# Kernel tuning notes

Measured on AMD Instinct MI355X. Metric: run time of the kernel, lower is better.

## Reference

```python
import jax, jax.numpy as jnp
import numpy as np
from jax import lax


def _conv(x, w, b):
    # x: [B,C,H,W], w: [O,I,3,3] (OIHW), SAME padding, stride 1
    y = lax.conv_general_dilated(x, w, (1, 1), 'SAME',
                                 dimension_numbers=('NCHW', 'OIHW', 'NCHW'))
    return y + b[None, :, None, None]


def _maxpool2(x):
    return lax.reduce_window(x, -jnp.inf, lax.max, (1, 1, 2, 2), (1, 1, 2, 2), 'VALID')


def setup_inputs() -> dict:
    key = jax.random.key(0)
    ks = iter(jax.random.split(key, 40))

    def conv_w(o, i):
        std = np.sqrt(2.0 / (9.0 * o)).astype(np.float32)  # kaiming as in _initialize_weights
        return jax.random.normal(next(ks), (o, i, 3, 3), jnp.float32) * std

    def lin_w(o, i):
        return jax.random.normal(next(ks), (o, i), jnp.float32) * 0.01

    inp = {
        'x': jax.random.normal(next(ks), (64, 3, 64, 64), jnp.float32),
        'y': jax.random.randint(next(ks), (64,), 0, 1000, dtype=jnp.int32),
        'b_table': jax.random.randint(next(ks), (1000, 128), 0, 512, dtype=jnp.int32),
        'cw0': conv_w(64, 3),    'cb0': jnp.zeros((64,), jnp.float32),
        'cw1': conv_w(128, 64),  'cb1': jnp.zeros((128,), jnp.float32),
        'cw2a': conv_w(256, 128), 'cb2a': jnp.zeros((256,), jnp.float32),
        'cw2b': conv_w(256, 256), 'cb2b': jnp.zeros((256,), jnp.float32),
        'cw3a': conv_w(512, 256), 'cb3a': jnp.zeros((512,), jnp.float32),
        'cw3b': conv_w(512, 512), 'cb3b': jnp.zeros((512,), jnp.float32),
        'cw4a': conv_w(512, 512), 'cb4a': jnp.zeros((512,), jnp.float32),
        'cw4b': conv_w(512, 512), 'cb4b': jnp.zeros((512,), jnp.float32),
        'fw1': lin_w(4096, 2048), 'fb1': jnp.zeros((4096,), jnp.float32),
        'fw2': lin_w(4096, 4096), 'fb2': jnp.zeros((4096,), jnp.float32),
        'fw3': lin_w(1000, 4096), 'fb3': jnp.zeros((1000,), jnp.float32),
    }
    return inp


def reference(x, y, b_table, cw0, cb0, cw1, cb1, cw2a, cb2a, cw2b, cb2b,
              cw3a, cb3a, cw3b, cb3b, cw4a, cb4a, cw4b, cb4b,
              fw1, fb1, fw2, fb2, fw3, fb3):
    B = x.shape[0]
    relu = jax.nn.relu
    # block0 (single conv, relu applied in forward)
    h = relu(_conv(x, cw0, cb0))
    h = _maxpool2(h)                       # 32x32
    # block1
    h = relu(_conv(h, cw1, cb1))
    h = _maxpool2(h)                       # 16x16
    # block2: conv, relu, conv (trailing relu stripped, applied in forward)
    h = relu(_conv(relu(_conv(h, cw2a, cb2a)), cw2b, cb2b))
    h = _maxpool2(h)                       # 8x8
    # block3
    h = relu(_conv(relu(_conv(h, cw3a, cb3a)), cw3b, cb3b))
    h = _maxpool2(h)                       # h==64 path: pool3 -> 4x4
    # block4
    h = relu(_conv(relu(_conv(h, cw4a, cb4a)), cw4b, cb4b))  # [B,512,4,4]

    # ---- engram channel masking (gather + sort + scatter) ----
    ranking = jnp.sort(b_table[y], axis=-1)            # [B, engram_number] channel ids
    mask = jnp.zeros((B, 512), h.dtype).at[jnp.arange(B)[:, None], ranking].set(1.0)
    h = h * mask[:, :, None, None]

    h = _maxpool2(h)                       # [B,512,2,2]
    h = h.reshape(B, -1)                   # [B,2048]
    # classifier (dropout = identity in eval mode)
    h = relu(h @ fw1.T + fb1)
    h = relu(h @ fw2.T + fb2)
    return h @ fw3.T + fb3                 # [B,1000]
```

## Files before the change

kernel.cpp:

```cpp
#include <hip/hip_runtime.h>
#include <hip/hip_bf16.h>
#include <cstddef>

typedef __attribute__((ext_vector_type(8))) short short8;
typedef __attribute__((ext_vector_type(4))) float fx4;
typedef __attribute__((ext_vector_type(4))) unsigned short us4;
typedef __attribute__((ext_vector_type(8))) unsigned short us8;

constexpr int BATCH = 64;

static __device__ __forceinline__ unsigned short f2bf(float x) {
    __hip_bfloat16 h = __float2bfloat16(x);
    return *reinterpret_cast<unsigned short*>(&h);
}

__global__ __launch_bounds__(256)
void conv0_kernel(const float* __restrict__ x, const float* __restrict__ w,
                  const float* __restrict__ bias, unsigned short* __restrict__ out)
{
    __shared__ float ins[3][18][19];
    const int tid  = threadIdx.x;
    const int lane = tid & 63;
    const int wv   = __builtin_amdgcn_readfirstlane(tid >> 6);
    const int img  = blockIdx.x >> 4;
    const int tile = blockIdx.x & 15;
    const int ty0  = (tile >> 2) * 16, tx0 = (tile & 3) * 16;
    const int py0  = (lane >> 3) * 2,  px0 = (lane & 7) * 2;
    const int co0  = wv * 16;

    for (int t = tid; t < 3*18*18; t += 256) {
        int xx = t % 18, yy = (t/18) % 18, ci = t/(18*18);
        int gy = ty0 + yy - 1, gx = tx0 + xx - 1;
        float v = 0.f;
        if (gy >= 0 && gy < 64 && gx >= 0 && gx < 64)
            v = x[((img*3 + ci)*64 + gy)*64 + gx];
        ins[ci][yy][xx] = v;
    }
    __syncthreads();

    float acc[16][4];
    #pragma unroll
    for (int j = 0; j < 16; j++)
        #pragma unroll
        for (int r = 0; r < 4; r++) acc[j][r] = 0.f;

    #pragma unroll
    for (int ci = 0; ci < 3; ci++) {
        float p[4][4];
        #pragma unroll
        for (int dy = 0; dy < 4; dy++)
            #pragma unroll
            for (int dx = 0; dx < 4; dx++)
                p[dy][dx] = ins[ci][py0+dy][px0+dx];
        #pragma unroll
        for (int j = 0; j < 16; j++) {
            const float* wp = w + ((co0+j)*3 + ci)*9;
            float w0=wp[0],w1=wp[1],w2=wp[2],w3=wp[3],w4=wp[4],
                  w5=wp[5],w6=wp[6],w7=wp[7],w8=wp[8];
            #pragma unroll
            for (int oy = 0; oy < 2; oy++)
                #pragma unroll
                for (int ox = 0; ox < 2; ox++)
                    acc[j][oy*2+ox] +=
                        p[oy+0][ox+0]*w0 + p[oy+0][ox+1]*w1 + p[oy+0][ox+2]*w2 +
                        p[oy+1][ox+0]*w3 + p[oy+1][ox+1]*w4 + p[oy+1][ox+2]*w5 +
                        p[oy+2][ox+0]*w6 + p[oy+2][ox+1]*w7 + p[oy+2][ox+2]*w8;
        }
    }

    us8 v0, v1;
    #pragma unroll
    for (int j = 0; j < 16; j++) {
        float m = fmaxf(fmaxf(acc[j][0], acc[j][1]), fmaxf(acc[j][2], acc[j][3]));
        unsigned short u = f2bf(fmaxf(m + bias[co0+j], 0.f));
        if (j < 8) v0[j] = u; else v1[j-8] = u;
    }
    int oy = (ty0+py0) >> 1, ox = (tx0+px0) >> 1;
    unsigned short* o = &out[((size_t)(img*32+oy)*32 + ox)*64 + co0];
    *(us8*)(o)     = v0;
    *(us8*)(o + 8) = v1;
}

struct PPAll {
    const float* src[7];
    unsigned long long dstoff[7];
    int cin[7];
    int cout[7];
    int end[7];
};

__global__ __launch_bounds__(256)
void prepack(PPAll a, unsigned short* __restrict__ wpbase)
{
    int t = blockIdx.x*256 + threadIdx.x;
    if (t >= 1024000) return;
    int l = 0;
    while (t >= a.end[l]) l++;
    int start = (l == 0) ? 0 : a.end[l-1];
    int local = t - start;
    int cin = a.cin[l], cout = a.cout[l];
    int co = local / cin, ci = local % cin;
    const float* s = a.src[l] + (size_t)local * 9;
    unsigned short* d = wpbase + a.dstoff[l];
    int kct = cin >> 5;
    #pragma unroll
    for (int k = 0; k < 9; k++)
        d[((size_t)(k*kct + (ci >> 5))*cout + co)*32 + (ci & 31)] = f2bf(s[k]);
}

template<int CIN, int COUT, int H, int CW, int SW, int P, int KS, bool POOL>
__global__ __launch_bounds__(256, 2)
void conv_mfma(const unsigned short* __restrict__ in, const unsigned short* __restrict__ wp,
               const float* __restrict__ bias, void* __restrict__ outp)
{
    constexpr int RY   = (P == 1) ? 8 : 4;
    constexpr int HY   = RY + 2, HX = RY + 2;
    constexpr int KCT  = CIN / 32;
    constexpr int CINS = CIN / KS;
    constexpr int KC   = CINS / 32;
    constexpr int PADW = (CINS == 128) ? 24 : 8;
    constexpr int STR  = CINS + PADW;
    constexpr int REG  = (P == 1) ? (H/8)*(H/8) : 1;
    static_assert(CW * SW == 4, "4 waves");

    __shared__ unsigned short ins[SW][P][HY][HX][STR];

    const int tid  = threadIdx.x;
    const int lane = tid & 63;
    const int wv   = __builtin_amdgcn_readfirstlane(tid >> 6);
    const int quad = lane >> 4;
    const int nn   = lane & 15;
    const int cg   = wv % CW;
    const int sg   = wv / CW;
    const int co0  = (blockIdx.y * CW + cg) * 64;
    const int ks   = (KS > 1) ? (int)blockIdx.z : 0;

    auto decode = [&](int rg, int& img, int& y0, int& x0) {
        if constexpr (P == 1) {
            img = rg / REG;
            int rs = rg % REG;
            constexpr int RXN = (P == 1) ? (H/8) : 1;
            y0 = (rs / RXN) * 8;
            x0 = (rs % RXN) * 8;
        } else {
            img = rg * 4; y0 = 0; x0 = 0;
        }
    };

    int w_img, w_y0, w_x0;
    decode(blockIdx.x * SW + sg, w_img, w_y0, w_x0);

    {
        constexpr int E = SW*P*HY*HX*(CINS/8);
        for (int u = tid; u < E; u += 256) {
            int q   = u % (CINS/8);
            int pix = u / (CINS/8);
            int xx  = pix % HX;
            int yy  = (pix / HX) % HY;
            int pp  = (pix / (HX*HY)) % P;
            int ss  = pix / (HX*HY*P);
            int s_img, s_y0, s_x0;
            decode(blockIdx.x * SW + ss, s_img, s_y0, s_x0);
            int gy = s_y0 + yy - 1, gx = s_x0 + xx - 1;
            int imgp = s_img + ((P == 1) ? 0 : pp);
            us8 v;
            #pragma unroll
            for (int e = 0; e < 8; e++) v[e] = 0;
            if (gy >= 0 && gy < H && gx >= 0 && gx < H)
                v = *(const us8*)&in[(((size_t)imgp*H + gy)*H + gx)*CIN + ks*CINS + q*8];
            *(us8*)&ins[ss][pp][yy][xx][q*8] = v;
        }
    }
    __syncthreads();

    fx4 acc[4][4];
    #pragma unroll
    for (int mf = 0; mf < 4; mf++)
        #pragma unroll
        for (int nf = 0; nf < 4; nf++) {
            fx4 z = {0.f, 0.f, 0.f, 0.f};
            acc[mf][nf] = z;
        }

    #pragma unroll 1
    for (int kc = 0; kc < KC; kc++) {
        #pragma unroll 3
        for (int tap = 0; tap < 9; tap++) {
            const int dy = tap / 3, dx = tap % 3;
            const unsigned short* wb =
                wp + ((size_t)(tap*KCT + ks*KC + kc)*COUT + co0 + nn)*32 + quad*8;
            short8 a[4];
            #pragma unroll
            for (int mf = 0; mf < 4; mf++)
                a[mf] = *(const short8*)(wb + (size_t)mf*16*32);
            short8 b[4];
            #pragma unroll
            for (int nf = 0; nf < 4; nf++) {
                int pp, py, px;
                if constexpr (P == 1) { pp = 0;  py = (nf>>1)*4 + (nn>>2); px = (nf&1)*4 + (nn&3); }
                else                  { pp = nf; py = (nn>>2);             px = (nn&3); }
                b[nf] = *(const short8*)&ins[sg][pp][py+dy][px+dx][kc*32 + quad*8];
            }
            #pragma unroll
            for (int mf = 0; mf < 4; mf++)
                #pragma unroll
                for (int nf = 0; nf < 4; nf++)
                    acc[mf][nf] = __builtin_amdgcn_mfma_f32_16x16x32_bf16(
                        a[mf], b[nf], acc[mf][nf], 0, 0, 0);
        }
    }

    if constexpr (KS > 1) {
        float* part = (float*)outp;
        constexpr size_t NPIX = (size_t)BATCH * H * H;
        #pragma unroll
        for (int mf = 0; mf < 4; mf++)
            #pragma unroll
            for (int nf = 0; nf < 4; nf++) {
                int img, py, px;
                if constexpr (P == 1) { img = w_img;      py = w_y0 + (nf>>1)*4 + (nn>>2); px = w_x0 + (nf&1)*4 + (nn&3); }
                else                  { img = w_img + nf; py = (nn>>2);                    px = (nn&3); }
                size_t npix = (size_t)img*H*H + py*H + px;
                size_t idx  = ((size_t)ks*NPIX + npix)*COUT + co0 + mf*16 + quad*4;
                *(fx4*)&part[idx] = acc[mf][nf];
            }
    } else if constexpr (POOL) {
        unsigned short* out = (unsigned short*)outp;
        constexpr int HO = H/2;
        #pragma unroll
        for (int mf = 0; mf < 4; mf++) {
            fx4 b4 = *(const fx4*)&bias[co0 + mf*16 + quad*4];
            #pragma unroll
            for (int nf = 0; nf < 4; nf++) {
                us4 o;
                #pragma unroll
                for (int r = 0; r < 4; r++) {
                    float v = acc[mf][nf][r];
                    v = fmaxf(v, __shfl_xor(v, 1));
                    v = fmaxf(v, __shfl_xor(v, 4));
                    o[r] = f2bf(fmaxf(v + b4[r], 0.f));
                }
                if ((nn & 5) == 0) {
                    int py = w_y0 + (nf>>1)*4 + (nn>>2);
                    int px = w_x0 + (nf&1)*4 + (nn&3);
                    size_t idx = (((size_t)w_img*HO + (py>>1))*HO + (px>>1))*COUT
                               + co0 + mf*16 + quad*4;
                    *(us4*)&out[idx] = o;
                }
            }
        }
    } else {
        unsigned short* out = (unsigned short*)outp;
        #pragma unroll
        for (int mf = 0; mf < 4; mf++) {
            fx4 b4 = *(const fx4*)&bias[co0 + mf*16 + quad*4];
            #pragma unroll
            for (int nf = 0; nf < 4; nf++) {
                us4 o;
                #pragma unroll
                for (int r = 0; r < 4; r++)
                    o[r] = f2bf(fmaxf(acc[mf][nf][r] + b4[r], 0.f));
                int py = w_y0 + (nf>>1)*4 + (nn>>2);
                int px = w_x0 + (nf&1)*4 + (nn&3);
                size_t idx = (((size_t)w_img*H + py)*H + px)*COUT + co0 + mf*16 + quad*4;
                *(us4*)&out[idx] = o;
            }
        }
    }
}

template<int KS, int NPIX, int CO>
__global__ __launch_bounds__(256)
void combine_nhwc(const float* __restrict__ part, const float* __restrict__ bias,
                  unsigned short* __restrict__ out)
{
    constexpr int C4 = CO/4;
    int t = blockIdx.x*256 + threadIdx.x;
    if (t >= NPIX*C4) return;
    int c4 = t % C4, pix = t / C4;
    fx4 s = *(const fx4*)&bias[c4*4];
    #pragma unroll
    for (int k = 0; k < KS; k++)
        s += *(const fx4*)&part[((size_t)k*NPIX + pix)*CO + c4*4];
    us4 o;
    #pragma unroll
    for (int r = 0; r < 4; r++) o[r] = f2bf(fmaxf(s[r], 0.f));
    *(us4*)&out[(size_t)pix*CO + c4*4] = o;
}

template<int KS, int HI, int CO>
__global__ __launch_bounds__(256)
void combine_pool(const float* __restrict__ part, const float* __restrict__ bias,
                  unsigned short* __restrict__ out)
{
    constexpr int HO = HI/2, C4 = CO/4;
    constexpr size_t NPIX = (size_t)BATCH*HI*HI;
    int t = blockIdx.x*256 + threadIdx.x;
    if (t >= BATCH*HO*HO*C4) return;
    int c4 = t % C4;
    int r  = t / C4;
    int xo = r % HO, yo = (r/HO) % HO, img = r/(HO*HO);
    fx4 m = {-1e30f, -1e30f, -1e30f, -1e30f};
    #pragma unroll
    for (int iy = 0; iy < 2; iy++)
        #pragma unroll
        for (int ix = 0; ix < 2; ix++) {
            size_t pix = (size_t)img*HI*HI + (2*yo+iy)*HI + (2*xo+ix);
            fx4 s = {0.f,0.f,0.f,0.f};
            #pragma unroll
            for (int k = 0; k < KS; k++)
                s += *(const fx4*)&part[((size_t)k*NPIX + pix)*CO + c4*4];
            #pragma unroll
            for (int e = 0; e < 4; e++) m[e] = fmaxf(m[e], s[e]);
        }
    fx4 b4 = *(const fx4*)&bias[c4*4];
    us4 o;
    #pragma unroll
    for (int e = 0; e < 4; e++) o[e] = f2bf(fmaxf(m[e] + b4[e], 0.f));
    *(us4*)&out[((size_t)(img*HO+yo)*HO + xo)*CO + c4*4] = o;
}

__global__ __launch_bounds__(256)
void combine4b(const float* __restrict__ part, const float* __restrict__ bias,
               const float* __restrict__ mask, unsigned short* __restrict__ X0)
{
    int t = blockIdx.x*256 + threadIdx.x;
    if (t >= BATCH*512) return;
    int b = t / 512, c = t % 512;
    float s[16];
    #pragma unroll
    for (int p = 0; p < 16; p++) s[p] = 0.f;
    #pragma unroll
    for (int k = 0; k < 16; k++)
        #pragma unroll
        for (int p = 0; p < 16; p++)
            s[p] += part[((size_t)k*1024 + b*16 + p)*512 + c];
    float mk = mask[b*512 + c], bb = bias[c];
    us4 o;
    #pragma unroll
    for (int py = 0; py < 2; py++)
        #pragma unroll
        for (int px = 0; px < 2; px++) {
            float m = fmaxf(fmaxf(s[(2*py)*4 + 2*px],     s[(2*py)*4 + 2*px+1]),
                            fmaxf(s[(2*py+1)*4 + 2*px],   s[(2*py+1)*4 + 2*px+1]));
            o[py*2+px] = f2bf(mk * fmaxf(m + bb, 0.f));
        }
    *(us4*)&X0[(size_t)b*2048 + c*4] = o;
}

__global__ void build_mask(const int* __restrict__ y, const int* __restrict__ btab,
                           float* __restrict__ mask)
{
    __shared__ float m[512];
    int b = blockIdx.x;
    int t = threadIdx.x;
    for (int i = t; i < 512; i += 128) m[i] = 0.f;
    __syncthreads();
    int cls = y[b];
    int idx = btab[cls*128 + t];
    m[idx] = 1.0f;
    __syncthreads();
    for (int i = t; i < 512; i += 128) mask[b*512 + i] = m[i];
}

template<int K, int NP, int NREAL, int KSO>
__global__ __launch_bounds__(256)
void fc_mfma(const unsigned short* __restrict__ X, const float* __restrict__ W,
             float* __restrict__ P)
{
    constexpr int KW = K / (KSO*4);
    constexpr int NI = KW / 32;
    __shared__ alignas(16) unsigned short XL[4][64][40];
    __shared__ alignas(16) float R[64][68];

    const int tid  = threadIdx.x;
    const int lane = tid & 63;
    const int wv   = __builtin_amdgcn_readfirstlane(tid >> 6);
    const int quad = lane >> 4;
    const int nn   = lane & 15;
    const int c0   = blockIdx.x * 64;
    const int ksb  = blockIdx.y;
    const int k0   = (ksb*4 + wv) * KW;

    fx4 acc[4][4];
    #pragma unroll
    for (int mf = 0; mf < 4; mf++)
        #pragma unroll
        for (int nf = 0; nf < 4; nf++) {
            fx4 z = {0.f,0.f,0.f,0.f};
            acc[mf][nf] = z;
        }

    #pragma unroll
    for (int kc = 0; kc < NI; kc++) {
        const int kw = k0 + kc*32;
        const unsigned short* xp = X + (size_t)lane*K + kw;
        us8 x0 = *(const us8*)(xp);
        us8 x1 = *(const us8*)(xp + 8);
        us8 x2 = *(const us8*)(xp + 16);
        us8 x3 = *(const us8*)(xp + 24);
        *(us8*)&XL[wv][lane][0]  = x0;
        *(us8*)&XL[wv][lane][8]  = x1;
        *(us8*)&XL[wv][lane][16] = x2;
        *(us8*)&XL[wv][lane][24] = x3;
        short8 b[4];
        #pragma unroll
        for (int nf = 0; nf < 4; nf++) {
            int c = c0 + nf*16 + nn;
            if (c > NREAL-1) c = NREAL-1;
            const float* wp = W + (size_t)c*K + kw + quad*8;
            float4 f0 = *(const float4*)(wp);
            float4 f1 = *(const float4*)(wp + 4);
            short8 t;
            t[0] = (short)f2bf(f0.x); t[1] = (short)f2bf(f0.y);
            t[2] = (short)f2bf(f0.z); t[3] = (short)f2bf(f0.w);
            t[4] = (short)f2bf(f1.x); t[5] = (short)f2bf(f1.y);
            t[6] = (short)f2bf(f1.z); t[7] = (short)f2bf(f1.w);
            b[nf] = t;
        }
        short8 a[4];
        #pragma unroll
        for (int mf = 0; mf < 4; mf++)
            a[mf] = *(const short8*)&XL[wv][mf*16 + nn][quad*8];
        #pragma unroll
        for (int mf = 0; mf < 4; mf++)
            #pragma unroll
            for (int nf = 0; nf < 4; nf++)
                acc[mf][nf] = __builtin_amdgcn_mfma_f32_16x16x32_bf16(
                    a[mf], b[nf], acc[mf][nf], 0, 0, 0);
    }

    for (int ww = 0; ww < 4; ww++) {
        __syncthreads();
        if (wv == ww) {
            #pragma unroll
            for (int mf = 0; mf < 4; mf++)
                #pragma unroll
                for (int nf = 0; nf < 4; nf++) {
                    int n = nf*16 + nn;
                    #pragma unroll
                    for (int r = 0; r < 4; r++) {
                        int m = mf*16 + quad*4 + r;
                        float v = acc[mf][nf][r];
                        if (ww) v += R[m][n];
                        R[m][n] = v;
                    }
                }
        }
    }
    __syncthreads();
    {
        int m  = tid >> 2;
        int n0 = (tid & 3) * 16;
        float* dst = P + ((size_t)ksb*64 + m)*NP + c0 + n0;
        #pragma unroll
        for (int j = 0; j < 4; j++) {
            fx4 v = *(const fx4*)&R[m][n0 + j*4];
            *(fx4*)(dst + j*4) = v;
        }
    }
}

template<int N, int KS>
__global__ __launch_bounds__(256)
void fc_combine_bf16(const float* __restrict__ P, const float* __restrict__ bias,
                     unsigned short* __restrict__ Xo)
{
    int t = blockIdx.x*256 + threadIdx.x;
    if (t >= 64*(N/4)) return;
    int c4 = t % (N/4);
    int b  = t / (N/4);
    fx4 s = *(const fx4*)&bias[c4*4];
    #pragma unroll
    for (int ks = 0; ks < KS; ks++)
        s += *(const fx4*)&P[((size_t)ks*64 + b)*N + c4*4];
    us4 o;
    #pragma unroll
    for (int r = 0; r < 4; r++) o[r] = f2bf(fmaxf(s[r], 0.f));
    *(us4*)&Xo[(size_t)b*N + c4*4] = o;
}

__global__ __launch_bounds__(256)
void fc3_combine(const float* __restrict__ P, const float* __restrict__ bias,
                 float* __restrict__ out)
{
    int t = blockIdx.x*256 + threadIdx.x;
    if (t >= 64*1000) return;
    int b = t / 1000, c = t % 1000;
    float s = bias[c];
    #pragma unroll
    for (int ks = 0; ks < 32; ks++)
        s += P[((size_t)ks*64 + b)*1024 + c];
    out[t] = s;
}

extern "C" void kernel_launch(void* const* d_in, const int* in_sizes, int n_in,
                              void* d_out, int out_size, void* d_ws, size_t ws_size,
                              hipStream_t stream)
{
    const float* x    = (const float*)d_in[0];
    const int*   y    = (const int*)  d_in[1];
    const int*   btab = (const int*)  d_in[2];
    const float* cw0  = (const float*)d_in[3];  const float* cb0  = (const float*)d_in[4];
    const float* cw1  = (const float*)d_in[5];  const float* cb1  = (const float*)d_in[6];
    const float* cw2a = (const float*)d_in[7];  const float* cb2a = (const float*)d_in[8];
    const float* cw2b = (const float*)d_in[9];  const float* cb2b = (const float*)d_in[10];
    const float* cw3a = (const float*)d_in[11]; const float* cb3a = (const float*)d_in[12];
    const float* cw3b = (const float*)d_in[13]; const float* cb3b = (const float*)d_in[14];
    const float* cw4a = (const float*)d_in[15]; const float* cb4a = (const float*)d_in[16];
    const float* cw4b = (const float*)d_in[17]; const float* cb4b = (const float*)d_in[18];
    const float* fw1  = (const float*)d_in[19]; const float* fb1  = (const float*)d_in[20];
    const float* fw2  = (const float*)d_in[21]; const float* fb2  = (const float*)d_in[22];
    const float* fw3  = (const float*)d_in[23]; const float* fb3  = (const float*)d_in[24];
    (void)in_sizes; (void)n_in; (void)out_size; (void)ws_size;

    float* ws = (float*)d_ws;
    unsigned short* ActA = (unsigned short*)(ws);
    unsigned short* ActB = (unsigned short*)(ws + 2097152);
    float*          Pp   = ws + 3145728;
    unsigned short* Wp   = (unsigned short*)(ws + 11534336);
    float*          M    = ws + 16142336;
    unsigned short* X0   = (unsigned short*)(ws + 16175104);
    unsigned short* X1   = (unsigned short*)(ws + 16240640);
    unsigned short* X2   = (unsigned short*)(ws + 16371712);

    PPAll pa;
    const float* srcs[7] = {cw1, cw2a, cw2b, cw3a, cw3b, cw4a, cw4b};
    const unsigned long long doffs[7] = {0, 73728, 368640, 958464, 2138112, 4497408, 6856704};
    const int cins[7]  = {64, 128, 256, 256, 512, 512, 512};
    const int couts[7] = {128, 256, 256, 512, 512, 512, 512};
    const int ends[7]  = {8192, 40960, 106496, 237568, 499712, 761856, 1024000};
    for (int i = 0; i < 7; i++) {
        pa.src[i] = srcs[i]; pa.dstoff[i] = doffs[i];
        pa.cin[i] = cins[i]; pa.cout[i] = couts[i]; pa.end[i] = ends[i];
    }
    prepack<<<4000, 256, 0, stream>>>(pa, Wp);

    conv0_kernel<<<1024, 256, 0, stream>>>(x, cw0, cb0, ActA);
    conv_mfma<64,128,32,2,2,1,1,true><<<dim3(512,1,1),256,0,stream>>>(ActA, Wp+0, cb1, ActB);
    conv_mfma<128,256,16,2,2,1,2,false><<<dim3(128,2,2),256,0,stream>>>(ActB, Wp+73728, cb2a, Pp);
    combine_nhwc<2, 16384, 256><<<4096,256,0,stream>>>(Pp, cb2a, ActA);
    conv_mfma<256,256,16,2,2,1,2,false><<<dim3(128,2,2),256,0,stream>>>(ActA, Wp+368640, cb2b, Pp);
    combine_pool<2, 16, 256><<<1024,256,0,stream>>>(Pp, cb2b, ActB);
    conv_mfma<256,512,8,4,1,1,4,false><<<dim3(64,2,4),256,0,stream>>>(ActB, Wp+958464, cb3a, Pp);
    combine_nhwc<4, 4096, 512><<<2048,256,0,stream>>>(Pp, cb3a, ActA);
    conv_mfma<512,512,8,4,1,1,4,false><<<dim3(64,2,4),256,0,stream>>>(ActA, Wp+2138112, cb3b, Pp);
    combine_pool<4, 8, 512><<<512,256,0,stream>>>(Pp, cb3b, ActB);
    conv_mfma<512,512,4,4,1,4,16,false><<<dim3(16,2,16),256,0,stream>>>(ActB, Wp+4497408, cb4a, Pp);
    combine_nhwc<16, 1024, 512><<<512,256,0,stream>>>(Pp, cb4a, ActA);
    build_mask<<<64,128,0,stream>>>(y, btab, M);
    conv_mfma<512,512,4,4,1,4,16,false><<<dim3(16,2,16),256,0,stream>>>(ActA, Wp+6856704, cb4b, Pp);
    combine4b<<<128,256,0,stream>>>(Pp, cb4b, M, X0);
    fc_mfma<2048,4096,4096,8><<<dim3(64,8),256,0,stream>>>(X0, fw1, Pp);
    fc_combine_bf16<4096,8><<<256,256,0,stream>>>(Pp, fb1, X1);
    fc_mfma<4096,4096,4096,8><<<dim3(64,8),256,0,stream>>>(X1, fw2, Pp);
    fc_combine_bf16<4096,8><<<256,256,0,stream>>>(Pp, fb2, X2);
    fc_mfma<4096,1024,1000,32><<<dim3(16,32),256,0,stream>>>(X2, fw3, Pp);
    fc3_combine<<<250,256,0,stream>>>(Pp, fb3, (float*)d_out);
}
```

Before: 516.3 us.

## Halve conv wave tile to 32 pixels, raise occupancy, add split-K pre-reduction

Result: slower. 537.0 us (+4.0%).

```diff
diff --git a/kernel.cpp b/kernel.cpp
--- a/kernel.cpp
+++ b/kernel.cpp
@@ -108,20 +108,19 @@
         d[((size_t)(k*kct + (ci >> 5))*cout + co)*32 + (ci & 31)] = f2bf(s[k]);
 }
 
-template<int CIN, int COUT, int H, int CW, int SW, int P, int KS, bool POOL>
-__global__ __launch_bounds__(256, 2)
+template<int CIN, int COUT, int H, int CW, int SW, int P, int RY, int RX, int KS, bool POOL>
+__global__ __launch_bounds__(256, 4)
 void conv_mfma(const unsigned short* __restrict__ in, const unsigned short* __restrict__ wp,
                const float* __restrict__ bias, void* __restrict__ outp)
 {
-    constexpr int RY   = (P == 1) ? 8 : 4;
-    constexpr int HY   = RY + 2, HX = RY + 2;
+    constexpr int HY   = RY + 2, HX = RX + 2;
     constexpr int KCT  = CIN / 32;
     constexpr int CINS = CIN / KS;
     constexpr int KC   = CINS / 32;
     constexpr int PADW = (CINS == 128) ? 24 : 8;
     constexpr int STR  = CINS + PADW;
-    constexpr int REG  = (P == 1) ? (H/8)*(H/8) : 1;
     static_assert(CW * SW == 4, "4 waves");
+    static_assert(P * RY * RX == 32, "N=32 wave tile");
 
     __shared__ unsigned short ins[SW][P][HY][HX][STR];
 
@@ -137,13 +136,14 @@
 
     auto decode = [&](int rg, int& img, int& y0, int& x0) {
         if constexpr (P == 1) {
+            constexpr int REG = (H/RY)*(H/RX);
+            constexpr int RXN = H/RX;
             img = rg / REG;
             int rs = rg % REG;
-            constexpr int RXN = (P == 1) ? (H/8) : 1;
-            y0 = (rs / RXN) * 8;
-            x0 = (rs % RXN) * 8;
+            y0 = (rs / RXN) * RY;
+            x0 = (rs % RXN) * RX;
         } else {
-            img = rg * 4; y0 = 0; x0 = 0;
+            img = rg * P; y0 = 0; x0 = 0;
         }
     };
 
@@ -173,11 +173,11 @@
     }
     __syncthreads();
 
-    fx4 acc[4][4];
+    fx4 acc[4][2];
     #pragma unroll
     for (int mf = 0; mf < 4; mf++)
         #pragma unroll
-        for (int nf = 0; nf < 4; nf++) {
+        for (int nf = 0; nf < 2; nf++) {
             fx4 z = {0.f, 0.f, 0.f, 0.f};
             acc[mf][nf] = z;
         }
@@ -193,18 +193,18 @@
             #pragma unroll
             for (int mf = 0; mf < 4; mf++)
                 a[mf] = *(const short8*)(wb + (size_t)mf*16*32);
-            short8 b[4];
-            #pragma unroll
-            for (int nf = 0; nf < 4; nf++) {
+            short8 b[2];
+            #pragma unroll
+            for (int nf = 0; nf < 2; nf++) {
                 int pp, py, px;
-                if constexpr (P == 1) { pp = 0;  py = (nf>>1)*4 + (nn>>2); px = (nf&1)*4 + (nn&3); }
-                else                  { pp = nf; py = (nn>>2);             px = (nn&3); }
+                if constexpr (P == 1) { pp = 0;  py = nf*4 + (nn>>2); px = nn & 3; }
+                else                  { pp = nf; py = nn>>2;          px = nn & 3; }
                 b[nf] = *(const short8*)&ins[sg][pp][py+dy][px+dx][kc*32 + quad*8];
             }
             #pragma unroll
             for (int mf = 0; mf < 4; mf++)
                 #pragma unroll
-                for (int nf = 0; nf < 4; nf++)
+                for (int nf = 0; nf < 2; nf++)
                     acc[mf][nf] = __builtin_amdgcn_mfma_f32_16x16x32_bf16(
                         a[mf], b[nf], acc[mf][nf], 0, 0, 0);
         }
@@ -216,10 +216,10 @@
         #pragma unroll
         for (int mf = 0; mf < 4; mf++)
             #pragma unroll
-            for (int nf = 0; nf < 4; nf++) {
+            for (int nf = 0; nf < 2; nf++) {
                 int img, py, px;
-                if constexpr (P == 1) { img = w_img;      py = w_y0 + (nf>>1)*4 + (nn>>2); px = w_x0 + (nf&1)*4 + (nn&3); }
-                else                  { img = w_img + nf; py = (nn>>2);                    px = (nn&3); }
+                if constexpr (P == 1) { img = w_img;      py = w_y0 + nf*4 + (nn>>2); px = w_x0 + (nn&3); }
+                else                  { img = w_img + nf; py = nn>>2;                 px = nn&3; }
                 size_t npix = (size_t)img*H*H + py*H + px;
                 size_t idx  = ((size_t)ks*NPIX + npix)*COUT + co0 + mf*16 + quad*4;
                 *(fx4*)&part[idx] = acc[mf][nf];
@@ -231,7 +231,7 @@
         for (int mf = 0; mf < 4; mf++) {
             fx4 b4 = *(const fx4*)&bias[co0 + mf*16 + quad*4];
             #pragma unroll
-            for (int nf = 0; nf < 4; nf++) {
+            for (int nf = 0; nf < 2; nf++) {
                 us4 o;
                 #pragma unroll
                 for (int r = 0; r < 4; r++) {
@@ -241,9 +241,10 @@
                     o[r] = f2bf(fmaxf(v + b4[r], 0.f));
                 }
                 if ((nn & 5) == 0) {
-                    int py = w_y0 + (nf>>1)*4 + (nn>>2);
-                    int px = w_x0 + (nf&1)*4 + (nn&3);
-                    size_t idx = (((size_t)w_img*HO + (py>>1))*HO + (px>>1))*COUT
+                    int img, py, px;
+                    if constexpr (P == 1) { img = w_img;      py = w_y0 + nf*4 + (nn>>2); px = w_x0 + (nn&3); }
+                    else                  { img = w_img + nf; py = nn>>2;                 px = nn&3; }
+                    size_t idx = (((size_t)img*HO + (py>>1))*HO + (px>>1))*COUT
                                + co0 + mf*16 + quad*4;
                     *(us4*)&out[idx] = o;
                 }
@@ -255,18 +256,34 @@
         for (int mf = 0; mf < 4; mf++) {
             fx4 b4 = *(const fx4*)&bias[co0 + mf*16 + quad*4];
             #pragma unroll
-            for (int nf = 0; nf < 4; nf++) {
+            for (int nf = 0; nf < 2; nf++) {
                 us4 o;
                 #pragma unroll
                 for (int r = 0; r < 4; r++)
                     o[r] = f2bf(fmaxf(acc[mf][nf][r] + b4[r], 0.f));
-                int py = w_y0 + (nf>>1)*4 + (nn>>2);
-                int px = w_x0 + (nf&1)*4 + (nn&3);
-                size_t idx = (((size_t)w_img*H + py)*H + px)*COUT + co0 + mf*16 + quad*4;
+                int img, py, px;
+                if constexpr (P == 1) { img = w_img;      py = w_y0 + nf*4 + (nn>>2); px = w_x0 + (nn&3); }
+                else                  { img = w_img + nf; py = nn>>2;                 px = nn&3; }
+                size_t idx = (((size_t)img*H + py)*H + px)*COUT + co0 + mf*16 + quad*4;
                 *(us4*)&out[idx] = o;
             }
         }
     }
+}
+
+template<int NELEM, int GROUPS, int STRIDE>
+__global__ __launch_bounds__(256)
+void ksum4(float* __restrict__ p)
+{
+    int t = blockIdx.x*256 + threadIdx.x;
+    if (t >= GROUPS*(NELEM/4)) return;
+    int g = t / (NELEM/4);
+    int i = (t % (NELEM/4)) * 4;
+    fx4 s = {0.f,0.f,0.f,0.f};
+    #pragma unroll
+    for (int j = 0; j < 4; j++)
+        s += *(const fx4*)&p[(size_t)((g*4 + j)*STRIDE)*NELEM + i];
+    *(fx4*)&p[(size_t)(g*4*STRIDE)*NELEM + i] = s;
 }
 
 template<int KS, int NPIX, int CO>
@@ -329,12 +346,8 @@
     int b = t / 512, c = t % 512;
     float s[16];
     #pragma unroll
-    for (int p = 0; p < 16; p++) s[p] = 0.f;
-    #pragma unroll
-    for (int k = 0; k < 16; k++)
-        #pragma unroll
-        for (int p = 0; p < 16; p++)
-            s[p] += part[((size_t)k*1024 + b*16 + p)*512 + c];
+    for (int p = 0; p < 16; p++)
+        s[p] = part[(size_t)(b*16 + p)*512 + c];
     float mk = mask[b*512 + c], bb = bias[c];
     us4 o;
     #pragma unroll
@@ -489,8 +502,8 @@
     int b = t / 1000, c = t % 1000;
     float s = bias[c];
     #pragma unroll
-    for (int ks = 0; ks < 32; ks++)
-        s += P[((size_t)ks*64 + b)*1024 + c];
+    for (int ks = 0; ks < 8; ks++)
+        s += P[((size_t)(ks*4)*64 + b)*1024 + c];
     out[t] = s;
 }
 
@@ -537,24 +550,30 @@
     prepack<<<4000, 256, 0, stream>>>(pa, Wp);
 
     conv0_kernel<<<1024, 256, 0, stream>>>(x, cw0, cb0, ActA);
-    conv_mfma<64,128,32,2,2,1,1,true><<<dim3(512,1,1),256,0,stream>>>(ActA, Wp+0, cb1, ActB);
-    conv_mfma<128,256,16,2,2,1,2,false><<<dim3(128,2,2),256,0,stream>>>(ActB, Wp+73728, cb2a, Pp);
+    conv_mfma<64,128,32,2,2,1,8,4,1,true><<<dim3(1024,1,1),256,0,stream>>>(ActA, Wp+0, cb1, ActB);
+    conv_mfma<128,256,16,2,2,1,8,4,2,false><<<dim3(256,2,2),256,0,stream>>>(ActB, Wp+73728, cb2a, Pp);
     combine_nhwc<2, 16384, 256><<<4096,256,0,stream>>>(Pp, cb2a, ActA);
-    conv_mfma<256,256,16,2,2,1,2,false><<<dim3(128,2,2),256,0,stream>>>(ActA, Wp+368640, cb2b, Pp);
+    conv_mfma<256,256,16,2,2,1,8,4,2,false><<<dim3(256,2,2),256,0,stream>>>(ActA, Wp+368640, cb2b, Pp);
     combine_pool<2, 16, 256><<<1024,256,0,stream>>>(Pp, cb2b, ActB);
-    conv_mfma<256,512,8,4,1,1,4,false><<<dim3(64,2,4),256,0,stream>>>(ActB, Wp+958464, cb3a, Pp);
+    conv_mfma<256,512,8,2,2,1,8,4,4,false><<<dim3(64,4,4),256,0,stream>>>(ActB, Wp+958464, cb3a, Pp);
     combine_nhwc<4, 4096, 512><<<2048,256,0,stream>>>(Pp, cb3a, ActA);
-    conv_mfma<512,512,8,4,1,1,4,false><<<dim3(64,2,4),256,0,stream>>>(ActA, Wp+2138112, cb3b, Pp);
-    combine_pool<4, 8, 512><<<512,256,0,stream>>>(Pp, cb3b, ActB);
-    conv_mfma<512,512,4,4,1,4,16,false><<<dim3(16,2,16),256,0,stream>>>(ActB, Wp+4497408, cb4a, Pp);
-    combine_nhwc<16, 1024, 512><<<512,256,0,stream>>>(Pp, cb4a, ActA);
+    conv_mfma<512,512,8,2,2,1,8,4,4,false><<<dim3(64,4,4),256,0,stream>>>(ActA, Wp+2138112, cb3b, Pp);
+    ksum4<2097152,1,1><<<2048,256,0,stream>>>(Pp);
+    combine_pool<1, 8, 512><<<512,256,0,stream>>>(Pp, cb3b, ActB);
+    conv_mfma<512,512,4,2,2,2,4,4,16,false><<<dim3(16,4,16),256,0,stream>>>(ActB, Wp+4497408, cb4a, Pp);
+    ksum4<524288,4,1><<<2048,256,0,stream>>>(Pp);
+    ksum4<524288,1,4><<<512,256,0,stream>>>(Pp);
+    combine_nhwc<1, 1024, 512><<<512,256,0,stream>>>(Pp, cb4a, ActA);
     build_mask<<<64,128,0,stream>>>(y, btab, M);
-    conv_mfma<512,512,4,4,1,4,16,false><<<dim3(16,2,16),256,0,stream>>>(ActA, Wp+6856704, cb4b, Pp);
+    conv_mfma<512,512,4,2,2,2,4,4,16,false><<<dim3(16,4,16),256,0,stream>>>(ActA, Wp+6856704, cb4b, Pp);
+    ksum4<524288,4,1><<<2048,256,0,stream>>>(Pp);
+    ksum4<524288,1,4><<<512,256,0,stream>>>(Pp);
     combine4b<<<128,256,0,stream>>>(Pp, cb4b, M, X0);
     fc_mfma<2048,4096,4096,8><<<dim3(64,8),256,0,stream>>>(X0, fw1, Pp);
     fc_combine_bf16<4096,8><<<256,256,0,stream>>>(Pp, fb1, X1);
     fc_mfma<4096,4096,4096,8><<<dim3(64,8),256,0,stream>>>(X1, fw2, Pp);
     fc_combine_bf16<4096,8><<<256,256,0,stream>>>(Pp, fb2, X2);
     fc_mfma<4096,1024,1000,32><<<dim3(16,32),256,0,stream>>>(X2, fw3, Pp);
+    ksum4<65536,8,1><<<512,256,0,stream>>>(Pp);
     fc3_combine<<<250,256,0,stream>>>(Pp, fb3, (float*)d_out);
 }
```
